# Kernel tuning notes

Measured on AMD Instinct MI355X. Metric: run time of the kernel, lower is better.

## Reference

```python
import jax, jax.numpy as jnp
import numpy as np

NUM_ITERATIONS = 3


def setup_inputs() -> dict:
    key = jax.random.key(0)
    k1, k2 = jax.random.split(key)
    B, I, C, U, D = 64, 8, 2048, 32, 16
    x = jax.random.normal(k1, (B, I, C), dtype=jnp.float32)
    # W matches torch param (1, C, U, D, I) with leading 1 squeezed
    W = jax.random.normal(k2, (C, U, D, I), dtype=jnp.float32)
    return {"x": x, "W": W}


def _squash(s):
    # Faithful to the original: reduction over axis 1 of s (B, U, D),
    # which corresponds to dim=2 of the torch tensor (B, 1, U, D, 1)
    # i.e. the num_units axis (quirk of the original code, reproduced).
    mag_sq = jnp.sum(s * s, axis=1, keepdims=True)  # (B, 1, D)
    mag = jnp.sqrt(mag_sq)
    return mag_sq / (1.0 + mag_sq) * (s / mag)


def reference(x, W):
    # x: (B, in_units, in_channels); W: (C, U, D, I)
    B = x.shape[0]
    x_t = jnp.transpose(x, (0, 2, 1))  # (B, C, I)
    # u_hat[b,c,u,d] = sum_i W[c,u,d,i] * x_t[b,c,i]
    u_hat = jnp.einsum("bci,cudi->bcud", x_t, W)  # (B, C, U, D)
    b_ij = jnp.zeros(W.shape[:2], dtype=u_hat.dtype)  # (C, U)
    v = None
    for _ in range(NUM_ITERATIONS):
        c_ij = jax.nn.softmax(b_ij, axis=1)  # softmax over num_units
        s_j = jnp.einsum("cu,bcud->bud", c_ij, u_hat)  # (B, U, D)
        v = _squash(s_j)  # (B, U, D)
        # agreement: dot over D, mean over batch -> (C, U)
        b_ij = b_ij + jnp.einsum("bcud,bud->cu", u_hat, v) / B
    # torch returns v_j.squeeze(1): shape (B, U, D, 1)
    return v[..., None]
```

## Files before the change

### kernel.cpp

```cpp
#include <hip/hip_runtime.h>

__device__ __forceinline__ void gload_lds16(const float* g, float* l) {
    __builtin_amdgcn_global_load_lds((const __attribute__((address_space(1))) void*)g,
                                     (__attribute__((address_space(3))) void*)l, 16, 0, 0);
}

__device__ __forceinline__ unsigned int f2bf1(float f) {
    union { float f; unsigned int u; } v; v.f = f;
    return (v.u + 0x7fffu + ((v.u >> 16) & 1u)) >> 16;
}
__device__ __forceinline__ unsigned int packbf(float a, float b) {
    return f2bf1(a) | (f2bf1(b) << 16);
}
__device__ __forceinline__ float2 bf2x(unsigned int p) {
    union { unsigned int u; float f; } lo, hi;
    lo.u = p << 16; hi.u = p & 0xffff0000u;
    return make_float2(lo.f, hi.f);
}

__global__ __launch_bounds__(256) void transpose_kernel(const float* __restrict__ x,
                                                        float* __restrict__ xt) {
    __shared__ float tile[64][65];
    const int bi0 = (blockIdx.x >> 5) << 6;
    const int c0  = (blockIdx.x & 31) << 6;
    const int tx = threadIdx.x & 63, ty = threadIdx.x >> 6;
#pragma unroll
    for (int p = 0; p < 16; ++p)
        tile[ty + p * 4][tx] = x[(size_t)(bi0 + ty + p * 4) * 2048 + c0 + tx];
    __syncthreads();
#pragma unroll
    for (int p = 0; p < 16; ++p) {
        int bi = bi0 + tx;
        xt[(size_t)(c0 + ty + p * 4) * 512 + (bi & 7) * 64 + (bi >> 3)] = tile[tx][ty + p * 4];
    }
}

template <int UNIFORM, int MODE>
__global__ __launch_bounds__(256) void s_kernel7(const float* __restrict__ xt,
                                                 const float* __restrict__ W,
                                                 unsigned short* __restrict__ Wb,
                                                 const float* __restrict__ cij,
                                                 float* __restrict__ part) {
    const int chunk = blockIdx.x >> 5;
    const int u     = blockIdx.x & 31;
    const int t = threadIdx.x, w = t >> 6, l = t & 63;
    const int dg = l >> 4, bq = l & 15;

    __shared__ float xbuf[8192];

    const int cbase = chunk * 64;
    float acc[16];
#pragma unroll
    for (int j = 0; j < 16; ++j) acc[j] = 0.f;

    {
        const float* g = xt + (size_t)cbase * 512 + w * 1024 + l * 4;
#pragma unroll
        for (int k = 0; k < 4; ++k)
            gload_lds16(g + k * 256, xbuf + w * 1024 + k * 256);
    }
    __syncthreads();

#pragma unroll 1
    for (int sl = 0; sl < 8; ++sl) {
        const int cur = (sl & 1) * 4096;
        if (sl < 7) {
            const int nxt = ((sl + 1) & 1) * 4096;
            const float* g = xt + (size_t)(cbase + (sl + 1) * 8) * 512 + w * 1024 + l * 4;
#pragma unroll
            for (int k = 0; k < 4; ++k)
                gload_lds16(g + k * 256, xbuf + nxt + w * 1024 + k * 256);
        }
#pragma unroll 1
        for (int j = 0; j < 2; ++j) {
            const int cl = w * 2 + j;
            const int c  = cbase + sl * 8 + cl;
            const float cw = UNIFORM ? 0.03125f : cij[c * 32 + u];
            const size_t wbase = ((size_t)c * 32 + u) * 128 + dg * 32;
            float4 wv[8];
            if (MODE == 2) {
                const uint4* Wp = reinterpret_cast<const uint4*>(Wb + wbase);
                unsigned int wu[16];
#pragma unroll
                for (int q = 0; q < 4; ++q) {
                    uint4 h = Wp[q];
                    wu[q * 4 + 0] = h.x; wu[q * 4 + 1] = h.y;
                    wu[q * 4 + 2] = h.z; wu[q * 4 + 3] = h.w;
                }
#pragma unroll
                for (int k = 0; k < 8; ++k) {
                    float2 a = bf2x(wu[2 * k]), b = bf2x(wu[2 * k + 1]);
                    wv[k] = make_float4(a.x, a.y, b.x, b.y);
                }
            } else {
                const float4* Wp = reinterpret_cast<const float4*>(W + wbase);
#pragma unroll
                for (int q = 0; q < 8; ++q) wv[q] = Wp[q];
                if (MODE == 1 && bq == 0) {
                    uint4* dst = reinterpret_cast<uint4*>(Wb + wbase);
#pragma unroll
                    for (int q = 0; q < 4; ++q) {
                        uint4 o;
                        o.x = packbf(wv[2 * q].x,     wv[2 * q].y);
                        o.y = packbf(wv[2 * q].z,     wv[2 * q].w);
                        o.z = packbf(wv[2 * q + 1].x, wv[2 * q + 1].y);
                        o.w = packbf(wv[2 * q + 1].z, wv[2 * q + 1].w);
                        dst[q] = o;
                    }
                }
            }
            float4 xv[8];
#pragma unroll
            for (int q = 0; q < 8; ++q)
                xv[q] = *reinterpret_cast<const float4*>(xbuf + cur + cl * 512 + q * 64 + bq * 4);
#pragma unroll
            for (int dd = 0; dd < 4; ++dd) {
                const float4 wa = wv[dd * 2], wb = wv[dd * 2 + 1];
                float uh0 = wa.x * xv[0].x + wa.y * xv[1].x + wa.z * xv[2].x + wa.w * xv[3].x
                          + wb.x * xv[4].x + wb.y * xv[5].x + wb.z * xv[6].x + wb.w * xv[7].x;
                float uh1 = wa.x * xv[0].y + wa.y * xv[1].y + wa.z * xv[2].y + wa.w * xv[3].y
                          + wb.x * xv[4].y + wb.y * xv[5].y + wb.z * xv[6].y + wb.w * xv[7].y;
                float uh2 = wa.x * xv[0].z + wa.y * xv[1].z + wa.z * xv[2].z + wa.w * xv[3].z
                          + wb.x * xv[4].z + wb.y * xv[5].z + wb.z * xv[6].z + wb.w * xv[7].z;
                float uh3 = wa.x * xv[0].w + wa.y * xv[1].w + wa.z * xv[2].w + wa.w * xv[3].w
                          + wb.x * xv[4].w + wb.y * xv[5].w + wb.z * xv[6].w + wb.w * xv[7].w;
                acc[dd * 4 + 0] += cw * uh0;
                acc[dd * 4 + 1] += cw * uh1;
                acc[dd * 4 + 2] += cw * uh2;
                acc[dd * 4 + 3] += cw * uh3;
            }
        }
        __syncthreads();
    }

#pragma unroll
    for (int j = 0; j < 16; ++j) xbuf[(w * 64 + l) * 17 + j] = acc[j];
    __syncthreads();
    const int l2 = t & 63, k = t >> 6;
    const int dg2 = l2 >> 4, bq2 = l2 & 15;
    float4 o;
    float* op = &o.x;
#pragma unroll
    for (int bb = 0; bb < 4; ++bb)
        op[bb] = xbuf[(0 * 64 + l2) * 17 + k * 4 + bb] + xbuf[(1 * 64 + l2) * 17 + k * 4 + bb]
               + xbuf[(2 * 64 + l2) * 17 + k * 4 + bb] + xbuf[(3 * 64 + l2) * 17 + k * 4 + bb];
    *reinterpret_cast<float4*>(part + (((size_t)chunk * 32 + u) * 16 + dg2 * 4 + k) * 64 + bq2 * 4) = o;
}

__global__ __launch_bounds__(256) void reduce_kernel(const float4* __restrict__ part4,
                                                     float4* __restrict__ s4) {
    int n = blockIdx.x * 256 + threadIdx.x;
    float4 a = part4[n];
#pragma unroll
    for (int k = 1; k < 32; ++k) {
        float4 b = part4[(size_t)k * 8192 + n];
        a.x += b.x; a.y += b.y; a.z += b.z; a.w += b.w;
    }
    s4[n] = a;
}

__global__ __launch_bounds__(256) void v_kernel2(const float* __restrict__ s,
                                                 float* __restrict__ v,
                                                 float* __restrict__ out) {
    int n = blockIdx.x * 256 + threadIdx.x;
    int b = n >> 4, d = n & 15;
    float sv[32];
    float msq = 0.f;
#pragma unroll
    for (int u = 0; u < 32; ++u) {
        sv[u] = s[(u * 16 + d) * 64 + b];
        msq += sv[u] * sv[u];
    }
    float scale = msq / ((1.f + msq) * sqrtf(msq));
#pragma unroll
    for (int u = 0; u < 32; ++u) {
        float val = sv[u] * scale;
        v[(b * 32 + u) * 16 + d] = val;
        out[(b * 32 + u) * 16 + d] = val;
    }
}

template <int FIRST, int WBF16>
__global__ __launch_bounds__(256) void delta_kernel6(const float* __restrict__ xt,
                                                     const float* __restrict__ W,
                                                     const unsigned short* __restrict__ Wb,
                                                     const float* __restrict__ v,
                                                     float* __restrict__ bij,
                                                     float* __restrict__ cij) {
    const int c0 = blockIdx.x * 2;
    const int t = threadIdx.x;
    __shared__ float xs[1024];
    __shared__ float sm[64];
    {
        const float4 vq = reinterpret_cast<const float4*>(xt + (size_t)c0 * 512)[t];
        const float* pf = &vq.x;
        const int k = t * 4;
#pragma unroll
        for (int j2 = 0; j2 < 4; ++j2) {
            int e = k + j2, cl = e >> 9, rem = e & 511, i = rem >> 6, b = rem & 63;
            xs[cl * 512 + b * 8 + i] = pf[j2];
        }
    }
    __syncthreads();
    const int u = t >> 3, d0 = (t & 7) * 2;
    float4 a00, a01, a10, a11, b00, b01, b10, b11;
    if (WBF16) {
        const uint4* W0 = reinterpret_cast<const uint4*>(Wb + ((size_t)c0 * 32 + u) * 128 + d0 * 8);
        const uint4* W1 = reinterpret_cast<const uint4*>(Wb + ((size_t)(c0 + 1) * 32 + u) * 128 + d0 * 8);
        uint4 h0 = W0[0], h1 = W0[1], h2 = W1[0], h3 = W1[1];
        float2 p;
        p = bf2x(h0.x); a00.x = p.x; a00.y = p.y;  p = bf2x(h0.y); a00.z = p.x; a00.w = p.y;
        p = bf2x(h0.z); a01.x = p.x; a01.y = p.y;  p = bf2x(h0.w); a01.z = p.x; a01.w = p.y;
        p = bf2x(h1.x); a10.x = p.x; a10.y = p.y;  p = bf2x(h1.y); a10.z = p.x; a10.w = p.y;
        p = bf2x(h1.z); a11.x = p.x; a11.y = p.y;  p = bf2x(h1.w); a11.z = p.x; a11.w = p.y;
        p = bf2x(h2.x); b00.x = p.x; b00.y = p.y;  p = bf2x(h2.y); b00.z = p.x; b00.w = p.y;
        p = bf2x(h2.z); b01.x = p.x; b01.y = p.y;  p = bf2x(h2.w); b01.z = p.x; b01.w = p.y;
        p = bf2x(h3.x); b10.x = p.x; b10.y = p.y;  p = bf2x(h3.y); b10.z = p.x; b10.w = p.y;
        p = bf2x(h3.z); b11.x = p.x; b11.y = p.y;  p = bf2x(h3.w); b11.z = p.x; b11.w = p.y;
    } else {
        const float4* W0 = reinterpret_cast<const float4*>(W + ((size_t)c0 * 32 + u) * 128 + d0 * 8);
        const float4* W1 = reinterpret_cast<const float4*>(W + ((size_t)(c0 + 1) * 32 + u) * 128 + d0 * 8);
        a00 = W0[0]; a01 = W0[1]; a10 = W0[2]; a11 = W0[3];
        b00 = W1[0]; b01 = W1[1]; b10 = W1[2]; b11 = W1[3];
    }
    float p0 = 0.f, p1 = 0.f;
#pragma unroll 4
    for (int b = 0; b < 64; ++b) {
        const float2 vv = *reinterpret_cast<const float2*>(v + (b * 32 + u) * 16 + d0);
        {
            const float4 xa = *reinterpret_cast<const float4*>(xs + b * 8);
            const float4 xb = *reinterpret_cast<const float4*>(xs + b * 8 + 4);
            float uh0 = a00.x * xa.x + a00.y * xa.y + a00.z * xa.z + a00.w * xa.w
                      + a01.x * xb.x + a01.y * xb.y + a01.z * xb.z + a01.w * xb.w;
            float uh1 = a10.x * xa.x + a10.y * xa.y + a10.z * xa.z + a10.w * xa.w
                      + a11.x * xb.x + a11.y * xb.y + a11.z * xb.z + a11.w * xb.w;
            p0 += uh0 * vv.x + uh1 * vv.y;
        }
        {
            const float4 xa = *reinterpret_cast<const float4*>(xs + 512 + b * 8);
            const float4 xb = *reinterpret_cast<const float4*>(xs + 512 + b * 8 + 4);
            float uh0 = b00.x * xa.x + b00.y * xa.y + b00.z * xa.z + b00.w * xa.w
                      + b01.x * xb.x + b01.y * xb.y + b01.z * xb.z + b01.w * xb.w;
            float uh1 = b10.x * xa.x + b10.y * xa.y + b10.z * xa.z + b10.w * xa.w
                      + b11.x * xb.x + b11.y * xb.y + b11.z * xb.z + b11.w * xb.w;
            p1 += uh0 * vv.x + uh1 * vv.y;
        }
    }
    p0 += __shfl_xor(p0, 1); p0 += __shfl_xor(p0, 2); p0 += __shfl_xor(p0, 4);
    p1 += __shfl_xor(p1, 1); p1 += __shfl_xor(p1, 2); p1 += __shfl_xor(p1, 4);
    if ((t & 7) == 0) {
        float r0 = p0 * (1.0f / 64.0f), r1 = p1 * (1.0f / 64.0f);
        if (!FIRST) { r0 += bij[c0 * 32 + u]; r1 += bij[(c0 + 1) * 32 + u]; }
        bij[c0 * 32 + u] = r0; bij[(c0 + 1) * 32 + u] = r1;
        sm[u] = r0; sm[32 + u] = r1;
    }
    __syncthreads();
    if (t < 64) {
        float val = sm[t];
        float m = val;
#pragma unroll
        for (int mask = 16; mask >= 1; mask >>= 1) m = fmaxf(m, __shfl_xor(m, mask));
        float e = expf(val - m);
        float ssum = e;
#pragma unroll
        for (int mask = 16; mask >= 1; mask >>= 1) ssum += __shfl_xor(ssum, mask);
        cij[(c0 + (t >> 5)) * 32 + (t & 31)] = e / ssum;
    }
}

extern "C" void kernel_launch(void* const* d_in, const int* in_sizes, int n_in,
                              void* d_out, int out_size, void* d_ws, size_t ws_size,
                              hipStream_t stream) {
    const float* x = (const float*)d_in[0];
    const float* W = (const float*)d_in[1];
    float* out = (float*)d_out;

    float* ws   = (float*)d_ws;
    float* xt   = ws;
    float* bij  = xt + 1048576;
    float* cij  = bij + 65536;
    float* s    = cij + 65536;
    float* v    = s + 32768;
    float* part = v + 32768;
    unsigned short* Wb = (unsigned short*)(part + 1048576);

    const bool BF = ws_size >= (size_t)(2293760 * 4) + (size_t)33554432 * 2;

    transpose_kernel<<<256, 256, 0, stream>>>(x, xt);

    if (BF) {
        s_kernel7<1, 1><<<1024, 256, 0, stream>>>(xt, W, Wb, cij, part);
        reduce_kernel<<<32, 256, 0, stream>>>((const float4*)part, (float4*)s);
        v_kernel2<<<4, 256, 0, stream>>>(s, v, out);
        delta_kernel6<1, 1><<<1024, 256, 0, stream>>>(xt, W, Wb, v, bij, cij);

        s_kernel7<0, 2><<<1024, 256, 0, stream>>>(xt, W, Wb, cij, part);
        reduce_kernel<<<32, 256, 0, stream>>>((const float4*)part, (float4*)s);
        v_kernel2<<<4, 256, 0, stream>>>(s, v, out);
        delta_kernel6<0, 1><<<1024, 256, 0, stream>>>(xt, W, Wb, v, bij, cij);

        s_kernel7<0, 2><<<1024, 256, 0, stream>>>(xt, W, Wb, cij, part);
        reduce_kernel<<<32, 256, 0, stream>>>((const float4*)part, (float4*)s);
        v_kernel2<<<4, 256, 0, stream>>>(s, v, out);
    } else {
        s_kernel7<1, 0><<<1024, 256, 0, stream>>>(xt, W, Wb, cij, part);
        reduce_kernel<<<32, 256, 0, stream>>>((const float4*)part, (float4*)s);
        v_kernel2<<<4, 256, 0, stream>>>(s, v, out);
        delta_kernel6<1, 0><<<1024, 256, 0, stream>>>(xt, W, Wb, v, bij, cij);

        s_kernel7<0, 0><<<1024, 256, 0, stream>>>(xt, W, Wb, cij, part);
        reduce_kernel<<<32, 256, 0, stream>>>((const float4*)part, (float4*)s);
        v_kernel2<<<4, 256, 0, stream>>>(s, v, out);
        delta_kernel6<0, 0><<<1024, 256, 0, stream>>>(xt, W, Wb, v, bij, cij);

        s_kernel7<0, 0><<<1024, 256, 0, stream>>>(xt, W, Wb, cij, part);
        reduce_kernel<<<32, 256, 0, stream>>>((const float4*)part, (float4*)s);
        v_kernel2<<<4, 256, 0, stream>>>(s, v, out);
    }
}
```

Before: 224.3 us.

## Halve per-block work in s and delta kernels to double grid size

```diff
diff --git a/kernel.cpp b/kernel.cpp
--- a/kernel.cpp
+++ b/kernel.cpp
@@ -36,7 +36,7 @@
 }
 
 template <int UNIFORM, int MODE>
-__global__ __launch_bounds__(256) void s_kernel7(const float* __restrict__ xt,
+__global__ __launch_bounds__(256) void s_kernel8(const float* __restrict__ xt,
                                                  const float* __restrict__ W,
                                                  unsigned short* __restrict__ Wb,
                                                  const float* __restrict__ cij,
@@ -46,95 +46,89 @@
     const int t = threadIdx.x, w = t >> 6, l = t & 63;
     const int dg = l >> 4, bq = l & 15;
 
-    __shared__ float xbuf[8192];
-
-    const int cbase = chunk * 64;
+    __shared__ float lds[4608];
+
+    const int cbase = chunk * 32;
     float acc[16];
 #pragma unroll
     for (int j = 0; j < 16; ++j) acc[j] = 0.f;
 
     {
-        const float* g = xt + (size_t)cbase * 512 + w * 1024 + l * 4;
-#pragma unroll
-        for (int k = 0; k < 4; ++k)
-            gload_lds16(g + k * 256, xbuf + w * 1024 + k * 256);
+        const float* g = xt + (size_t)(cbase + w) * 512 + l * 4;
+        gload_lds16(g,       lds + w * 512);
+        gload_lds16(g + 256, lds + w * 512 + 256);
     }
     __syncthreads();
 
 #pragma unroll 1
     for (int sl = 0; sl < 8; ++sl) {
-        const int cur = (sl & 1) * 4096;
+        const int cur = (sl & 1) * 2048;
         if (sl < 7) {
-            const int nxt = ((sl + 1) & 1) * 4096;
-            const float* g = xt + (size_t)(cbase + (sl + 1) * 8) * 512 + w * 1024 + l * 4;
-#pragma unroll
-            for (int k = 0; k < 4; ++k)
-                gload_lds16(g + k * 256, xbuf + nxt + w * 1024 + k * 256);
-        }
-#pragma unroll 1
-        for (int j = 0; j < 2; ++j) {
-            const int cl = w * 2 + j;
-            const int c  = cbase + sl * 8 + cl;
-            const float cw = UNIFORM ? 0.03125f : cij[c * 32 + u];
-            const size_t wbase = ((size_t)c * 32 + u) * 128 + dg * 32;
-            float4 wv[8];
-            if (MODE == 2) {
-                const uint4* Wp = reinterpret_cast<const uint4*>(Wb + wbase);
-                unsigned int wu[16];
+            const int nxt = ((sl + 1) & 1) * 2048;
+            const float* g = xt + (size_t)(cbase + (sl + 1) * 4 + w) * 512 + l * 4;
+            gload_lds16(g,       lds + nxt + w * 512);
+            gload_lds16(g + 256, lds + nxt + w * 512 + 256);
+        }
+        const int c = cbase + sl * 4 + w;
+        const float cw = UNIFORM ? 0.03125f : cij[c * 32 + u];
+        const size_t wbase = ((size_t)c * 32 + u) * 128 + dg * 32;
+        float4 wv[8];
+        if (MODE == 2) {
+            const uint4* Wp = reinterpret_cast<const uint4*>(Wb + wbase);
+            unsigned int wu[16];
+#pragma unroll
+            for (int q = 0; q < 4; ++q) {
+                uint4 h = Wp[q];
+                wu[q * 4 + 0] = h.x; wu[q * 4 + 1] = h.y;
+                wu[q * 4 + 2] = h.z; wu[q * 4 + 3] = h.w;
+            }
+#pragma unroll
+            for (int k = 0; k < 8; ++k) {
+                float2 a = bf2x(wu[2 * k]), b = bf2x(wu[2 * k + 1]);
+                wv[k] = make_float4(a.x, a.y, b.x, b.y);
+            }
+        } else {
+            const float4* Wp = reinterpret_cast<const float4*>(W + wbase);
+#pragma unroll
+            for (int q = 0; q < 8; ++q) wv[q] = Wp[q];
+            if (MODE == 1 && bq == 0) {
+                uint4* dst = reinterpret_cast<uint4*>(Wb + wbase);
 #pragma unroll
                 for (int q = 0; q < 4; ++q) {
-                    uint4 h = Wp[q];
-                    wu[q * 4 + 0] = h.x; wu[q * 4 + 1] = h.y;
-                    wu[q * 4 + 2] = h.z; wu[q * 4 + 3] = h.w;
-                }
-#pragma unroll
-                for (int k = 0; k < 8; ++k) {
-                    float2 a = bf2x(wu[2 * k]), b = bf2x(wu[2 * k + 1]);
-                    wv[k] = make_float4(a.x, a.y, b.x, b.y);
-                }
-            } else {
-                const float4* Wp = reinterpret_cast<const float4*>(W + wbase);
-#pragma unroll
-                for (int q = 0; q < 8; ++q) wv[q] = Wp[q];
-                if (MODE == 1 && bq == 0) {
-                    uint4* dst = reinterpret_cast<uint4*>(Wb + wbase);
-#pragma unroll
-                    for (int q = 0; q < 4; ++q) {
-                        uint4 o;
-                        o.x = packbf(wv[2 * q].x,     wv[2 * q].y);
-                        o.y = packbf(wv[2 * q].z,     wv[2 * q].w);
-                        o.z = packbf(wv[2 * q + 1].x, wv[2 * q + 1].y);
-                        o.w = packbf(wv[2 * q + 1].z, wv[2 * q + 1].w);
-                        dst[q] = o;
-                    }
+                    uint4 o;
+                    o.x = packbf(wv[2 * q].x,     wv[2 * q].y);
+                    o.y = packbf(wv[2 * q].z,     wv[2 * q].w);
+                    o.z = packbf(wv[2 * q + 1].x, wv[2 * q + 1].y);
+                    o.w = packbf(wv[2 * q + 1].z, wv[2 * q + 1].w);
+                    dst[q] = o;
                 }
             }
-            float4 xv[8];
-#pragma unroll
-            for (int q = 0; q < 8; ++q)
-                xv[q] = *reinterpret_cast<const float4*>(xbuf + cur + cl * 512 + q * 64 + bq * 4);
-#pragma unroll
-            for (int dd = 0; dd < 4; ++dd) {
-                const float4 wa = wv[dd * 2], wb = wv[dd * 2 + 1];
-                float uh0 = wa.x * xv[0].x + wa.y * xv[1].x + wa.z * xv[2].x + wa.w * xv[3].x
-                          + wb.x * xv[4].x + wb.y * xv[5].x + wb.z * xv[6].x + wb.w * xv[7].x;
-                float uh1 = wa.x * xv[0].y + wa.y * xv[1].y + wa.z * xv[2].y + wa.w * xv[3].y
-                          + wb.x * xv[4].y + wb.y * xv[5].y + wb.z * xv[6].y + wb.w * xv[7].y;
-                float uh2 = wa.x * xv[0].z + wa.y * xv[1].z + wa.z * xv[2].z + wa.w * xv[3].z
-                          + wb.x * xv[4].z + wb.y * xv[5].z + wb.z * xv[6].z + wb.w * xv[7].z;
-                float uh3 = wa.x * xv[0].w + wa.y * xv[1].w + wa.z * xv[2].w + wa.w * xv[3].w
-                          + wb.x * xv[4].w + wb.y * xv[5].w + wb.z * xv[6].w + wb.w * xv[7].w;
-                acc[dd * 4 + 0] += cw * uh0;
-                acc[dd * 4 + 1] += cw * uh1;
-                acc[dd * 4 + 2] += cw * uh2;
-                acc[dd * 4 + 3] += cw * uh3;
-            }
+        }
+        float4 xv[8];
+#pragma unroll
+        for (int q = 0; q < 8; ++q)
+            xv[q] = *reinterpret_cast<const float4*>(lds + cur + w * 512 + q * 64 + bq * 4);
+#pragma unroll
+        for (int dd = 0; dd < 4; ++dd) {
+            const float4 wa = wv[dd * 2], wb = wv[dd * 2 + 1];
+            float uh0 = wa.x * xv[0].x + wa.y * xv[1].x + wa.z * xv[2].x + wa.w * xv[3].x
+                      + wb.x * xv[4].x + wb.y * xv[5].x + wb.z * xv[6].x + wb.w * xv[7].x;
+            float uh1 = wa.x * xv[0].y + wa.y * xv[1].y + wa.z * xv[2].y + wa.w * xv[3].y
+                      + wb.x * xv[4].y + wb.y * xv[5].y + wb.z * xv[6].y + wb.w * xv[7].y;
+            float uh2 = wa.x * xv[0].z + wa.y * xv[1].z + wa.z * xv[2].z + wa.w * xv[3].z
+                      + wb.x * xv[4].z + wb.y * xv[5].z + wb.z * xv[6].z + wb.w * xv[7].z;
+            float uh3 = wa.x * xv[0].w + wa.y * xv[1].w + wa.z * xv[2].w + wa.w * xv[3].w
+                      + wb.x * xv[4].w + wb.y * xv[5].w + wb.z * xv[6].w + wb.w * xv[7].w;
+            acc[dd * 4 + 0] += cw * uh0;
+            acc[dd * 4 + 1] += cw * uh1;
+            acc[dd * 4 + 2] += cw * uh2;
+            acc[dd * 4 + 3] += cw * uh3;
         }
         __syncthreads();
     }
 
 #pragma unroll
-    for (int j = 0; j < 16; ++j) xbuf[(w * 64 + l) * 17 + j] = acc[j];
+    for (int j = 0; j < 16; ++j) lds[(w * 64 + l) * 17 + j] = acc[j];
     __syncthreads();
     const int l2 = t & 63, k = t >> 6;
     const int dg2 = l2 >> 4, bq2 = l2 & 15;
@@ -142,8 +136,8 @@
     float* op = &o.x;
 #pragma unroll
     for (int bb = 0; bb < 4; ++bb)
-        op[bb] = xbuf[(0 * 64 + l2) * 17 + k * 4 + bb] + xbuf[(1 * 64 + l2) * 17 + k * 4 + bb]
-               + xbuf[(2 * 64 + l2) * 17 + k * 4 + bb] + xbuf[(3 * 64 + l2) * 17 + k * 4 + bb];
+        op[bb] = lds[(0 * 64 + l2) * 17 + k * 4 + bb] + lds[(1 * 64 + l2) * 17 + k * 4 + bb]
+               + lds[(2 * 64 + l2) * 17 + k * 4 + bb] + lds[(3 * 64 + l2) * 17 + k * 4 + bb];
     *reinterpret_cast<float4*>(part + (((size_t)chunk * 32 + u) * 16 + dg2 * 4 + k) * 64 + bq2 * 4) = o;
 }
 
@@ -152,7 +146,7 @@
     int n = blockIdx.x * 256 + threadIdx.x;
     float4 a = part4[n];
 #pragma unroll
-    for (int k = 1; k < 32; ++k) {
+    for (int k = 1; k < 64; ++k) {
         float4 b = part4[(size_t)k * 8192 + n];
         a.x += b.x; a.y += b.y; a.z += b.z; a.w += b.w;
     }
@@ -181,53 +175,42 @@
 }
 
 template <int FIRST, int WBF16>
-__global__ __launch_bounds__(256) void delta_kernel6(const float* __restrict__ xt,
+__global__ __launch_bounds__(256) void delta_kernel8(const float* __restrict__ xt,
                                                      const float* __restrict__ W,
                                                      const unsigned short* __restrict__ Wb,
                                                      const float* __restrict__ v,
                                                      float* __restrict__ bij,
                                                      float* __restrict__ cij) {
-    const int c0 = blockIdx.x * 2;
+    const int c = blockIdx.x;
     const int t = threadIdx.x;
-    __shared__ float xs[1024];
-    __shared__ float sm[64];
+    __shared__ float xs[512];
+    __shared__ float sm[32];
     {
-        const float4 vq = reinterpret_cast<const float4*>(xt + (size_t)c0 * 512)[t];
-        const float* pf = &vq.x;
-        const int k = t * 4;
-#pragma unroll
-        for (int j2 = 0; j2 < 4; ++j2) {
-            int e = k + j2, cl = e >> 9, rem = e & 511, i = rem >> 6, b = rem & 63;
-            xs[cl * 512 + b * 8 + i] = pf[j2];
-        }
+        const float2 vq = reinterpret_cast<const float2*>(xt + (size_t)c * 512)[t];
+        int e0 = t * 2, e1 = t * 2 + 1;
+        xs[(e0 & 63) * 8 + (e0 >> 6)] = vq.x;
+        xs[(e1 & 63) * 8 + (e1 >> 6)] = vq.y;
     }
     __syncthreads();
     const int u = t >> 3, d0 = (t & 7) * 2;
-    float4 a00, a01, a10, a11, b00, b01, b10, b11;
+    float4 a00, a01, a10, a11;
     if (WBF16) {
-        const uint4* W0 = reinterpret_cast<const uint4*>(Wb + ((size_t)c0 * 32 + u) * 128 + d0 * 8);
-        const uint4* W1 = reinterpret_cast<const uint4*>(Wb + ((size_t)(c0 + 1) * 32 + u) * 128 + d0 * 8);
-        uint4 h0 = W0[0], h1 = W0[1], h2 = W1[0], h3 = W1[1];
+        const uint4* W0 = reinterpret_cast<const uint4*>(Wb + ((size_t)c * 32 + u) * 128 + d0 * 8);
+        uint4 h0 = W0[0], h1 = W0[1];
         float2 p;
         p = bf2x(h0.x); a00.x = p.x; a00.y = p.y;  p = bf2x(h0.y); a00.z = p.x; a00.w = p.y;
         p = bf2x(h0.z); a01.x = p.x; a01.y = p.y;  p = bf2x(h0.w); a01.z = p.x; a01.w = p.y;
         p = bf2x(h1.x); a10.x = p.x; a10.y = p.y;  p = bf2x(h1.y); a10.z = p.x; a10.w = p.y;
         p = bf2x(h1.z); a11.x = p.x; a11.y = p.y;  p = bf2x(h1.w); a11.z = p.x; a11.w = p.y;
-        p = bf2x(h2.x); b00.x = p.x; b00.y = p.y;  p = bf2x(h2.y); b00.z = p.x; b00.w = p.y;
-        p = bf2x(h2.z); b01.x = p.x; b01.y = p.y;  p = bf2x(h2.w); b01.z = p.x; b01.w = p.y;
-        p = bf2x(h3.x); b10.x = p.x; b10.y = p.y;  p = bf2x(h3.y); b10.z = p.x; b10.w = p.y;
-        p = bf2x(h3.z); b11.x = p.x; b11.y = p.y;  p = bf2x(h3.w); b11.z = p.x; b11.w = p.y;
     } else {
-        const float4* W0 = reinterpret_cast<const float4*>(W + ((size_t)c0 * 32 + u) * 128 + d0 * 8);
-        const float4* W1 = reinterpret_cast<const float4*>(W + ((size_t)(c0 + 1) * 32 + u) * 128 + d0 * 8);
+        const float4* W0 = reinterpret_cast<const float4*>(W + ((size_t)c * 32 + u) * 128 + d0 * 8);
         a00 = W0[0]; a01 = W0[1]; a10 = W0[2]; a11 = W0[3];
-        b00 = W1[0]; b01 = W1[1]; b10 = W1[2]; b11 = W1[3];
     }
     float p0 = 0.f, p1 = 0.f;
 #pragma unroll 4
-    for (int b = 0; b < 64; ++b) {
-        const float2 vv = *reinterpret_cast<const float2*>(v + (b * 32 + u) * 16 + d0);
+    for (int b = 0; b < 64; b += 2) {
         {
+            const float2 vv = *reinterpret_cast<const float2*>(v + (b * 32 + u) * 16 + d0);
             const float4 xa = *reinterpret_cast<const float4*>(xs + b * 8);
             const float4 xb = *reinterpret_cast<const float4*>(xs + b * 8 + 4);
             float uh0 = a00.x * xa.x + a00.y * xa.y + a00.z * xa.z + a00.w * xa.w
@@ -237,25 +220,28 @@
             p0 += uh0 * vv.x + uh1 * vv.y;
         }
         {
-            const float4 xa = *reinterpret_cast<const float4*>(xs + 512 + b * 8);
-            const float4 xb = *reinterpret_cast<const float4*>(xs + 512 + b * 8 + 4);
-            float uh0 = b00.x * xa.x + b00.y * xa.y + b00.z * xa.z + b00.w * xa.w
-                      + b01.x * xb.x + b01.y * xb.y + b01.z * xb.z + b01.w * xb.w;
-            float uh1 = b10.x * xa.x + b10.y * xa.y + b10.z * xa.z + b10.w * xa.w
-                      + b11.x * xb.x + b11.y * xb.y + b11.z * xb.z + b11.w * xb.w;
+            const float2 vv = *reinterpret_cast<const float2*>(v + ((b + 1) * 32 + u) * 16 + d0);
+            const float4 xa = *reinterpret_cast<const float4*>(xs + (b + 1) * 8);
+            const float4 xb = *reinterpret_cast<const float4*>(xs + (b + 1) * 8 + 4);
+            float uh0 = a00.x * xa.x + a00.y * xa.y + a00.z * xa.z + a00.w * xa.w
+                      + a01.x * xb.x + a01.y * xb.y + a01.z * xb.z + a01.w * xb.w;
+            float uh1 = a10.x * xa.x + a10.y * xa.y + a10.z * xa.z + a10.w * xa.w
+                      + a11.x * xb.x + a11.y * xb.y + a11.z * xb.z + a11.w * xb.w;
             p1 += uh0 * vv.x + uh1 * vv.y;
         }
     }
-    p0 += __shfl_xor(p0, 1); p0 += __shfl_xor(p0, 2); p0 += __shfl_xor(p0, 4);
-    p1 += __shfl_xor(p1, 1); p1 += __shfl_xor(p1, 2); p1 += __shfl_xor(p1, 4);
+    float partial = p0 + p1;
+    partial += __shfl_xor(partial, 1);
+    partial += __shfl_xor(partial, 2);
+    partial += __shfl_xor(partial, 4);
     if ((t & 7) == 0) {
-        float r0 = p0 * (1.0f / 64.0f), r1 = p1 * (1.0f / 64.0f);
-        if (!FIRST) { r0 += bij[c0 * 32 + u]; r1 += bij[(c0 + 1) * 32 + u]; }
-        bij[c0 * 32 + u] = r0; bij[(c0 + 1) * 32 + u] = r1;
-        sm[u] = r0; sm[32 + u] = r1;
-    }
-    __syncthreads();
-    if (t < 64) {
+        float r = partial * (1.0f / 64.0f);
+        if (!FIRST) r += bij[c * 32 + u];
+        bij[c * 32 + u] = r;
+        sm[u] = r;
+    }
+    __syncthreads();
+    if (t < 32) {
         float val = sm[t];
         float m = val;
 #pragma unroll
@@ -264,7 +250,7 @@
         float ssum = e;
 #pragma unroll
         for (int mask = 16; mask >= 1; mask >>= 1) ssum += __shfl_xor(ssum, mask);
-        cij[(c0 + (t >> 5)) * 32 + (t & 31)] = e / ssum;
+        cij[c * 32 + t] = e / ssum;
     }
 }
 
@@ -282,39 +268,39 @@
     float* s    = cij + 65536;
     float* v    = s + 32768;
     float* part = v + 32768;
-    unsigned short* Wb = (unsigned short*)(part + 1048576);
-
-    const bool BF = ws_size >= (size_t)(2293760 * 4) + (size_t)33554432 * 2;
+    unsigned short* Wb = (unsigned short*)(part + 2097152);
+
+    const bool BF = ws_size >= (size_t)3342336 * 4 + (size_t)33554432 * 2;
 
     transpose_kernel<<<256, 256, 0, stream>>>(x, xt);
 
     if (BF) {
-        s_kernel7<1, 1><<<1024, 256, 0, stream>>>(xt, W, Wb, cij, part);
-        reduce_kernel<<<32, 256, 0, stream>>>((const float4*)part, (float4*)s);
-        v_kernel2<<<4, 256, 0, stream>>>(s, v, out);
-        delta_kernel6<1, 1><<<1024, 256, 0, stream>>>(xt, W, Wb, v, bij, cij);
-
-        s_kernel7<0, 2><<<1024, 256, 0, stream>>>(xt, W, Wb, cij, part);
-        reduce_kernel<<<32, 256, 0, stream>>>((const float4*)part, (float4*)s);
-        v_kernel2<<<4, 256, 0, stream>>>(s, v, out);
-        delta_kernel6<0, 1><<<1024, 256, 0, stream>>>(xt, W, Wb, v, bij, cij);
-
-        s_kernel7<0, 2><<<1024, 256, 0, stream>>>(xt, W, Wb, cij, part);
+        s_kernel8<1, 1><<<2048, 256, 0, stream>>>(xt, W, Wb, cij, part);
+        reduce_kernel<<<32, 256, 0, stream>>>((const float4*)part, (float4*)s);
+        v_kernel2<<<4, 256, 0, stream>>>(s, v, out);
+        delta_kernel8<1, 1><<<2048, 256, 0, stream>>>(xt, W, Wb, v, bij, cij);
+
+        s_kernel8<0, 2><<<2048, 256, 0, stream>>>(xt, W, Wb, cij, part);
+        reduce_kernel<<<32, 256, 0, stream>>>((const float4*)part, (float4*)s);
+        v_kernel2<<<4, 256, 0, stream>>>(s, v, out);
+        delta_kernel8<0, 1><<<2048, 256, 0, stream>>>(xt, W, Wb, v, bij, cij);
+
+        s_kernel8<0, 2><<<2048, 256, 0, stream>>>(xt, W, Wb, cij, part);
         reduce_kernel<<<32, 256, 0, stream>>>((const float4*)part, (float4*)s);
         v_kernel2<<<4, 256, 0, stream>>>(s, v, out);
     } else {
-        s_kernel7<1, 0><<<1024, 256, 0, stream>>>(xt, W, Wb, cij, part);
-        reduce_kernel<<<32, 256, 0, stream>>>((const float4*)part, (float4*)s);
-        v_kernel2<<<4, 256, 0, stream>>>(s, v, out);
-        delta_kernel6<1, 0><<<1024, 256, 0, stream>>>(xt, W, Wb, v, bij, cij);
-
-        s_kernel7<0, 0><<<1024, 256, 0, stream>>>(xt, W, Wb, cij, part);
-        reduce_kernel<<<32, 256, 0, stream>>>((const float4*)part, (float4*)s);
-        v_kernel2<<<4, 256, 0, stream>>>(s, v, out);
-        delta_kernel6<0, 0><<<1024, 256, 0, stream>>>(xt, W, Wb, v, bij, cij);
-
-        s_kernel7<0, 0><<<1024, 256, 0, stream>>>(xt, W, Wb, cij, part);
-        reduce_kernel<<<32, 256, 0, stream>>>((const float4*)part, (float4*)s);
-        v_kernel2<<<4, 256, 0, stream>>>(s, v, out);
-    }
-}
+        s_kernel8<1, 0><<<2048, 256, 0, stream>>>(xt, W, Wb, cij, part);
+        reduce_kernel<<<32, 256, 0, stream>>>((const float4*)part, (float4*)s);
+        v_kernel2<<<4, 256, 0, stream>>>(s, v, out);
+        delta_kernel8<1, 0><<<2048, 256, 0, stream>>>(xt, W, Wb, v, bij, cij);
+
+        s_kernel8<0, 0><<<2048, 256, 0, stream>>>(xt, W, Wb, cij, part);
+        reduce_kernel<<<32, 256, 0, stream>>>((const float4*)part, (float4*)s);
+        v_kernel2<<<4, 256, 0, stream>>>(s, v, out);
+        delta_kernel8<0, 0><<<2048, 256, 0, stream>>>(xt, W, Wb, v, bij, cij);
+
+        s_kernel8<0, 0><<<2048, 256, 0, stream>>>(xt, W, Wb, cij, part);
+        reduce_kernel<<<32, 256, 0, stream>>>((const float4*)part, (float4*)s);
+        v_kernel2<<<4, 256, 0, stream>>>(s, v, out);
+    }
+}
```

New measurement: 237.8 us. +6.0%, slower.
